# Kernel tuning notes

Hardware: AMD Instinct MI355X
Metric: run time of the kernel (lower is better)

The kernel has to match this reference:

```python
import jax, jax.numpy as jnp
import numpy as np

N, K, C, S = 40000, 16, 128, 8  # points, neighbors, channels, share_planes
EPS = 1e-5


def _bn(x, g, b, m, v):
    # eval-mode BatchNorm1d over the channel (last) axis
    return (x - m) * (g * jax.lax.rsqrt(v + EPS)) + b


def _forward(xyz, feats, Wq, bq, Wk, bk, Wv, bv, Wp1, bp1, p_gamma, p_beta, p_mean, p_var,
             Wp2, bp2, w_gamma, w_beta, w_mean, w_var, Ww1, bw1, w1_gamma, w1_beta,
             w1_mean, w1_var, Ww2, bw2, nei_ind):
    x = feats[0]          # (N, C)
    pos = xyz[0]          # (N, 3)
    idx = nei_ind[0]      # (N, K)

    q = x @ Wq + bq                      # (N, C)
    kf = (x @ Wk + bk)[idx]              # (N, K, C) neighbor gather
    vf = (x @ Wv + bv)[idx]              # (N, K, C)

    d = pos[idx] - pos[:, None, :]       # (N, K, 3) relative positions
    # linear_p: Linear_BN(3,3) -> ReLU -> Linear(3, C)
    p = jax.nn.relu(_bn(d @ Wp1 + bp1, p_gamma, p_beta, p_mean, p_var)) @ Wp2 + bp2  # (N, K, C)

    # mid_planes == out_planes, so the view(...,1,mid).sum(2) is an identity reshape
    w = kf - q[:, None, :] + p           # (N, K, C)
    w = _bn(w, w_gamma, w_beta, w_mean, w_var)  # bn_w over channels
    # linear_w: ReLU -> Linear_BN(C, C//S) -> ReLU -> Linear(C//S, C//S)
    w = jax.nn.relu(_bn(jax.nn.relu(w) @ Ww1 + bw1, w1_gamma, w1_beta, w1_mean, w1_var)) @ Ww2 + bw2  # (N, K, C//S)
    w = jax.nn.softmax(w, axis=1)        # softmax over K neighbors

    # grouped-channel weighted sum over neighbors
    agg = ((vf + p).reshape(N, K, S, C // S) * w[:, :, None, :]).sum(axis=1).reshape(N, C)

    # shortcut is Identity (in_planes == out_planes); broadcast over batch dim like torch
    return jax.nn.leaky_relu(agg[None, :, :] + feats, negative_slope=0.1)  # (1, N, C)


def setup_inputs() -> dict:
    key = jax.random.key(0)
    ks = jax.random.split(key, 16)
    f32 = jnp.float32

    def w(k, shape, scale):
        return jax.random.normal(k, shape, dtype=f32) * scale

    return {
        "xyz": jax.random.uniform(ks[0], (1, N, 3), dtype=f32),
        "feats": jax.random.normal(ks[1], (1, N, C), dtype=f32),
        "nei_ind": jax.random.randint(ks[2], (1, N, K), 0, N, dtype=jnp.int32),
        "Wq": w(ks[3], (C, C), C ** -0.5), "bq": jnp.zeros((C,), f32),
        "Wk": w(ks[4], (C, C), C ** -0.5), "bk": jnp.zeros((C,), f32),
        "Wv": w(ks[5], (C, C), C ** -0.5), "bv": jnp.zeros((C,), f32),
        "Wp1": w(ks[6], (3, 3), 0.5), "bp1": jnp.zeros((3,), f32),
        "p_gamma": jnp.ones((3,), f32), "p_beta": jnp.zeros((3,), f32),
        "p_mean": w(ks[7], (3,), 0.1), "p_var": jnp.ones((3,), f32),
        "Wp2": w(ks[8], (3, C), 0.5), "bp2": jnp.zeros((C,), f32),
        "w_gamma": jnp.ones((C,), f32), "w_beta": jnp.zeros((C,), f32),
        "w_mean": w(ks[9], (C,), 0.1), "w_var": jnp.ones((C,), f32),
        "Ww1": w(ks[10], (C, C // S), C ** -0.5), "bw1": jnp.zeros((C // S,), f32),
        "w1_gamma": jnp.ones((C // S,), f32), "w1_beta": jnp.zeros((C // S,), f32),
        "w1_mean": w(ks[11], (C // S,), 0.1), "w1_var": jnp.ones((C // S,), f32),
        "Ww2": w(ks[12], (C // S, C // S), (C // S) ** -0.5), "bw2": jnp.zeros((C // S,), f32),
    }


def reference(xyz, feats, nei_ind, Wq, bq, Wk, bk, Wv, bv, Wp1, bp1, p_gamma, p_beta,
              p_mean, p_var, Wp2, bp2, w_gamma, w_beta, w_mean, w_var, Ww1, bw1,
              w1_gamma, w1_beta, w1_mean, w1_var, Ww2, bw2):
    return _forward(xyz, feats, Wq, bq, Wk, bk, Wv, bv, Wp1, bp1, p_gamma, p_beta,
                    p_mean, p_var, Wp2, bp2, w_gamma, w_beta, w_mean, w_var, Ww1, bw1,
                    w1_gamma, w1_beta, w1_mean, w1_var, Ww2, bw2, nei_ind)
```

## Files before the change

### kernel.cpp

```cpp
#include <hip/hip_runtime.h>
#include <stdint.h>

#define N_PTS 40000
#define KNBR  16
#define CH    128
#define EPSV  1e-5f

typedef __attribute__((ext_vector_type(4))) float f32x4;
typedef __attribute__((ext_vector_type(8))) short bf16x8;

__device__ __forceinline__ float bf2f(ushort u) {
    union { uint32_t i; float f; } x; x.i = ((uint32_t)u) << 16; return x.f;
}
__device__ __forceinline__ float bflo(uint32_t u) {
    union { uint32_t i; float f; } x; x.i = u << 16; return x.f;
}
__device__ __forceinline__ float bfhi(uint32_t u) {
    union { uint32_t i; float f; } x; x.i = u & 0xffff0000u; return x.f;
}
__device__ __forceinline__ ushort f2bf(float f) {
    union { float f; uint32_t i; } x; x.f = f;
    uint32_t i = x.i;
    i += 0x7fffu + ((i >> 16) & 1u);
    return (ushort)(i >> 16);
}

#if __has_builtin(__builtin_amdgcn_cvt_pk_bf16_f32)
typedef __bf16 bf16x2v __attribute__((ext_vector_type(2)));
__device__ __forceinline__ uint32_t pack2(float a, float b) {
    union { bf16x2v v; uint32_t u; } x;
    x.v = __builtin_amdgcn_cvt_pk_bf16_f32(a, b);
    return x.u;
}
#else
__device__ __forceinline__ uint32_t pack2(float a, float b) {
    return (uint32_t)f2bf(a) | ((uint32_t)f2bf(b) << 16);
}
#endif

template <bool BF> struct IO;
template <> struct IO<true> {
    static __device__ __forceinline__ float  ld (const void* p, int i) { return bf2f(((const ushort*)p)[i]); }
    static __device__ __forceinline__ float2 ld2(const void* p, int i) { const uint32_t u = ((const uint32_t*)p)[i]; return make_float2(bflo(u), bfhi(u)); }
    static __device__ __forceinline__ ushort ldbf(const void* p, int i) { return ((const ushort*)p)[i]; }
    static __device__ __forceinline__ void   st2(void* p, int i, float a, float b) { ((uint32_t*)p)[i] = pack2(a, b); }
};
template <> struct IO<false> {
    static __device__ __forceinline__ float  ld (const void* p, int i) { return ((const float*)p)[i]; }
    static __device__ __forceinline__ float2 ld2(const void* p, int i) { return ((const float2*)p)[i]; }
    static __device__ __forceinline__ ushort ldbf(const void* p, int i) { return f2bf(((const float*)p)[i]); }
    static __device__ __forceinline__ void   st2(void* p, int i, float a, float b) { ((float2*)p)[i] = make_float2(a, b); }
};

__device__ __forceinline__ bool detect_bf16(const void* w_var) {
    return (*(const uint32_t*)w_var & 0xffffu) != 0u;
}

#define PROJ_BLOCKS 1250
template <bool BF>
__device__ void proj_body(
    const void* feats,
    const void* Wq, const void* bq, const void* Wk, const void* bk,
    const void* Wv, const void* bv,
    uint32_t* qws, uint4* kvws)
{
    const int l    = threadIdx.x & 63;
    const int w    = threadIdx.x >> 6;
    const int t    = l & 15;
    const int quad = l >> 4;
    const int cq   = w;

    const void* Wsrc[3] = { Wq, Wk, Wv };
    const void* bsrc[3] = { bq, bk, bv };

    bf16x8 afrag[3][4];
    float  bias[3][4];
    #pragma unroll
    for (int m = 0; m < 3; ++m) {
        #pragma unroll
        for (int s = 0; s < 4; ++s)
            #pragma unroll
            for (int j = 0; j < 8; ++j) {
                const int k = s * 32 + quad * 8 + j;
                afrag[m][s][j] = (short)IO<BF>::ldbf(Wsrc[m], k * CH + cq * 16 + t);
            }
        #pragma unroll
        for (int r = 0; r < 4; ++r)
            bias[m][r] = IO<BF>::ld(bsrc[m], cq * 16 + quad * 4 + r);
    }

    #pragma unroll
    for (int n = 0; n < 2; ++n) {
        const int tt = blockIdx.x + PROJ_BLOCKS * n;
        const int p0 = tt * 16;
        bf16x8 bfr[4];
        if (BF) {
            const ushort* xp = (const ushort*)feats + (p0 + t) * CH + quad * 8;
            #pragma unroll
            for (int s = 0; s < 4; ++s)
                bfr[s] = *(const bf16x8*)(xp + s * 32);
        } else {
            const float* xp = (const float*)feats + (p0 + t) * CH + quad * 8;
            #pragma unroll
            for (int s = 0; s < 4; ++s) {
                const float4 a = *(const float4*)(xp + s * 32);
                const float4 b = *(const float4*)(xp + s * 32 + 4);
                bfr[s][0] = (short)f2bf(a.x); bfr[s][1] = (short)f2bf(a.y);
                bfr[s][2] = (short)f2bf(a.z); bfr[s][3] = (short)f2bf(a.w);
                bfr[s][4] = (short)f2bf(b.x); bfr[s][5] = (short)f2bf(b.y);
                bfr[s][6] = (short)f2bf(b.z); bfr[s][7] = (short)f2bf(b.w);
            }
        }
        f32x4 acc[3];
        #pragma unroll
        for (int m = 0; m < 3; ++m) {
            acc[m] = f32x4{ bias[m][0], bias[m][1], bias[m][2], bias[m][3] };
            #pragma unroll
            for (int s = 0; s < 4; ++s)
                acc[m] = __builtin_amdgcn_mfma_f32_16x16x32_bf16(afrag[m][s], bfr[s], acc[m], 0, 0, 0);
        }
        const int p = p0 + t;
        const int m16 = cq * 4 + quad;
        uint2 qo;
        qo.x = pack2(acc[0][0], acc[0][1]);
        qo.y = pack2(acc[0][2], acc[0][3]);
        ((uint2*)qws)[p * 32 + m16] = qo;
        uint4 kv;
        kv.x = pack2(acc[1][0], acc[1][1]);
        kv.y = pack2(acc[2][0], acc[2][1]);
        kv.z = pack2(acc[1][2], acc[1][3]);
        kv.w = pack2(acc[2][2], acc[2][3]);
        kvws[p * 32 + m16] = kv;
    }
}

__global__ __launch_bounds__(512) void proj_kernel(
    const void* feats, const void* Wq, const void* bq, const void* Wk,
    const void* bk, const void* Wv, const void* bv, const void* w_var_probe,
    uint32_t* qws, uint4* kvws)
{
    if (detect_bf16(w_var_probe))
        proj_body<true >(feats, Wq, bq, Wk, bk, Wv, bv, qws, kvws);
    else
        proj_body<false>(feats, Wq, bq, Wk, bk, Wv, bv, qws, kvws);
}

template <bool BF>
__device__ void attn_body(
    const void* xyz, const void* feats, const int* __restrict__ nei,
    const uint32_t* __restrict__ qws, const uint2* __restrict__ kvws,
    const void* Wp1, const void* bp1, const void* p_gamma, const void* p_beta,
    const void* p_mean, const void* p_var, const void* Wp2, const void* bp2,
    const void* w_gamma, const void* w_beta, const void* w_mean, const void* w_var,
    const void* Ww1, const void* bw1, const void* w1_gamma, const void* w1_beta,
    const void* w1_mean, const void* w1_var, const void* Ww2, const void* bw2,
    void* out, ushort* wbuf, ushort* ubuf, float* wsm, float* hlds,
    int i0, int l)
{
    const int t = l & 15;
    const int quad = l >> 4;

    float A1[3][3], C1[3];
    #pragma unroll
    for (int b = 0; b < 3; ++b) {
        const float sb = IO<BF>::ld(p_gamma, b) * rsqrtf(IO<BF>::ld(p_var, b) + EPSV);
        C1[b] = (IO<BF>::ld(bp1, b) - IO<BF>::ld(p_mean, b)) * sb + IO<BF>::ld(p_beta, b);
        #pragma unroll
        for (int a = 0; a < 3; ++a) A1[a][b] = IO<BF>::ld(Wp1, a * 3 + b) * sb;
    }

    const float2 vg = IO<BF>::ld2(w_gamma, l);
    const float2 vb = IO<BF>::ld2(w_beta, l);
    const float2 vm = IO<BF>::ld2(w_mean, l);
    const float2 vv = IO<BF>::ld2(w_var, l);
    const float scw0 = vg.x * rsqrtf(vv.x + EPSV);
    const float scw1 = vg.y * rsqrtf(vv.y + EPSV);
    const float shw0 = vb.x - vm.x * scw0;
    const float shw1 = vb.y - vm.y * scw1;

    float wp2c[3][2];
    #pragma unroll
    for (int r = 0; r < 3; ++r) {
        const float2 u = IO<BF>::ld2(Wp2, r * 64 + l);
        wp2c[r][0] = u.x; wp2c[r][1] = u.y;
    }
    const float2 vbp2 = IO<BF>::ld2(bp2, l);
    const float bp20 = vbp2.x, bp21 = vbp2.y;

    bf16x8 bfrag1[4];
    #pragma unroll
    for (int s = 0; s < 4; ++s)
        #pragma unroll
        for (int kk = 0; kk < 8; ++kk) {
            const int k = s * 32 + quad * 8 + kk;
            bfrag1[s][kk] = (short)IO<BF>::ldbf(Ww1, k * 16 + t);
        }
    bf16x8 bfrag2;
    #pragma unroll
    for (int kk = 0; kk < 8; ++kk) {
        const int k = quad * 8 + kk;
        bfrag2[kk] = (quad < 2) ? (short)IO<BF>::ldbf(Ww2, k * 16 + t) : (short)0;
    }

    const float s1t  = IO<BF>::ld(w1_gamma, t) * rsqrtf(IO<BF>::ld(w1_var, t) + EPSV);
    const float sh1t = IO<BF>::ld(w1_beta, t) - IO<BF>::ld(w1_mean, t) * s1t;
    const float bw1t = IO<BF>::ld(bw1, t);
    const float bw2t = IO<BF>::ld(bw2, t);

    #pragma unroll 1
    for (int pp = 0; pp < 4; ++pp) {
        const int i = i0 + pp;

        const uint32_t uq = qws[i * 64 + l];
        const float qs0 = shw0 - bflo(uq) * scw0;
        const float qs1 = shw1 - bfhi(uq) * scw1;

        const float pix = IO<BF>::ld(xyz, i * 3 + 0);
        const float piy = IO<BF>::ld(xyz, i * 3 + 1);
        const float piz = IO<BF>::ld(xyz, i * 3 + 2);

        const int vnj = nei[i * KNBR + t];
        const float ndx = IO<BF>::ld(xyz, vnj * 3 + 0) - pix;
        const float ndy = IO<BF>::ld(xyz, vnj * 3 + 1) - piy;
        const float ndz = IO<BF>::ld(xyz, vnj * 3 + 2) - piz;
        const float hh0 = fmaxf(0.f, ndx * A1[0][0] + ndy * A1[1][0] + ndz * A1[2][0] + C1[0]);
        const float hh1 = fmaxf(0.f, ndx * A1[0][1] + ndy * A1[1][1] + ndz * A1[2][1] + C1[1]);
        const float hh2 = fmaxf(0.f, ndx * A1[0][2] + ndy * A1[1][2] + ndz * A1[2][2] + C1[2]);
        if (quad == 0)
            *(float4*)&hlds[t * 4] = make_float4(hh0, hh1, hh2, 0.f);

        int njs[KNBR];
        #pragma unroll
        for (int j = 0; j < KNBR; ++j) njs[j] = nei[i * KNBR + j];
        uint2 kv[KNBR];
        #pragma unroll
        for (int j = 0; j < KNBR; ++j) kv[j] = kvws[njs[j] * 64 + l];

        float vfp0[KNBR], vfp1[KNBR];
        #pragma unroll
        for (int j = 0; j < KNBR; ++j) {
            const float4 h = *(const float4*)&hlds[j * 4];
            const float p0 = h.x * wp2c[0][0] + h.y * wp2c[1][0] + h.z * wp2c[2][0] + bp20;
            const float p1 = h.x * wp2c[0][1] + h.y * wp2c[1][1] + h.z * wp2c[2][1] + bp21;
            vfp0[j] = bflo(kv[j].y) + p0;
            vfp1[j] = bfhi(kv[j].y) + p1;
            const float w0 = fmaxf(0.f, fmaf(bflo(kv[j].x) + p0, scw0, qs0));
            const float w1 = fmaxf(0.f, fmaf(bfhi(kv[j].x) + p1, scw1, qs1));
            ((uint32_t*)wbuf)[j * 68 + l] = pack2(w0, w1);
        }

        f32x4 acc1 = { bw1t, bw1t, bw1t, bw1t };
        const ushort* arow = &wbuf[t * 136 + quad * 8];
        #pragma unroll
        for (int s = 0; s < 4; ++s) {
            const bf16x8 afrag = *(const bf16x8*)(arow + s * 32);
            acc1 = __builtin_amdgcn_mfma_f32_16x16x32_bf16(afrag, bfrag1[s], acc1, 0, 0, 0);
        }
        #pragma unroll
        for (int r = 0; r < 4; ++r) {
            const float u = fmaxf(0.f, acc1[r] * s1t + sh1t);
            ubuf[(quad * 4 + r) * 24 + t] = f2bf(u);
        }

        f32x4 acc2 = { bw2t, bw2t, bw2t, bw2t };
        bf16x8 afrag2;
        if (quad < 2) {
            afrag2 = *(const bf16x8*)(&ubuf[t * 24 + quad * 8]);
        } else {
            #pragma unroll
            for (int kk = 0; kk < 8; ++kk) afrag2[kk] = 0;
        }
        acc2 = __builtin_amdgcn_mfma_f32_16x16x32_bf16(afrag2, bfrag2, acc2, 0, 0, 0);

        float z0 = acc2[0], z1 = acc2[1], z2 = acc2[2], z3 = acc2[3];
        float mx = fmaxf(fmaxf(z0, z1), fmaxf(z2, z3));
        mx = fmaxf(mx, __shfl_xor(mx, 16));
        mx = fmaxf(mx, __shfl_xor(mx, 32));
        const float e0 = __expf(z0 - mx), e1 = __expf(z1 - mx);
        const float e2 = __expf(z2 - mx), e3 = __expf(z3 - mx);
        float ssum = e0 + e1 + e2 + e3;
        ssum += __shfl_xor(ssum, 16);
        ssum += __shfl_xor(ssum, 32);
        const float inv = 1.0f / ssum;
        wsm[(quad * 4 + 0) * 18 + t] = e0 * inv;
        wsm[(quad * 4 + 1) * 18 + t] = e1 * inv;
        wsm[(quad * 4 + 2) * 18 + t] = e2 * inv;
        wsm[(quad * 4 + 3) * 18 + t] = e3 * inv;

        const int t0 = (2 * l) & 15;
        float agg0 = 0.f, agg1 = 0.f;
        #pragma unroll
        for (int j = 0; j < KNBR; ++j) {
            const float2 wp = *(const float2*)&wsm[j * 18 + t0];
            agg0 = fmaf(vfp0[j], wp.x, agg0);
            agg1 = fmaf(vfp1[j], wp.y, agg1);
        }
        const float2 xf = IO<BF>::ld2(feats, i * 64 + l);
        float o0 = agg0 + xf.x;
        float o1 = agg1 + xf.y;
        o0 = o0 > 0.f ? o0 : 0.1f * o0;
        o1 = o1 > 0.f ? o1 : 0.1f * o1;
        IO<BF>::st2(out, i * 64 + l, o0, o1);
    }
}

__global__ __launch_bounds__(256) void attn_kernel(
    const void* xyz, const void* feats, const int* __restrict__ nei,
    const uint32_t* __restrict__ qws, const uint2* __restrict__ kvws,
    const void* Wp1, const void* bp1, const void* p_gamma, const void* p_beta,
    const void* p_mean, const void* p_var, const void* Wp2, const void* bp2,
    const void* w_gamma, const void* w_beta, const void* w_mean, const void* w_var,
    const void* Ww1, const void* bw1, const void* w1_gamma, const void* w1_beta,
    const void* w1_mean, const void* w1_var, const void* Ww2, const void* bw2,
    void* out)
{
    __shared__ ushort wbuf[4][16 * 136];
    __shared__ ushort ubuf[4][16 * 24];
    __shared__ float  wsm [4][16 * 18];
    __shared__ float  hlds[4][16 * 4];

    const int wave = threadIdx.x >> 6;
    const int l    = threadIdx.x & 63;
    const int i0   = blockIdx.x * 16 + wave * 4;

    if (detect_bf16(w_var))
        attn_body<true >(xyz, feats, nei, qws, kvws, Wp1, bp1, p_gamma, p_beta,
                         p_mean, p_var, Wp2, bp2, w_gamma, w_beta, w_mean, w_var,
                         Ww1, bw1, w1_gamma, w1_beta, w1_mean, w1_var, Ww2, bw2,
                         out, wbuf[wave], ubuf[wave], wsm[wave], hlds[wave], i0, l);
    else
        attn_body<false>(xyz, feats, nei, qws, kvws, Wp1, bp1, p_gamma, p_beta,
                         p_mean, p_var, Wp2, bp2, w_gamma, w_beta, w_mean, w_var,
                         Ww1, bw1, w1_gamma, w1_beta, w1_mean, w1_var, Ww2, bw2,
                         out, wbuf[wave], ubuf[wave], wsm[wave], hlds[wave], i0, l);
}

extern "C" void kernel_launch(void* const* d_in, const int* in_sizes, int n_in,
                              void* d_out, int out_size, void* d_ws, size_t ws_size,
                              hipStream_t stream) {
    const void* xyz     = d_in[0];
    const void* feats   = d_in[1];
    const int*  nei     = (const int*)d_in[2];
    const void* Wq      = d_in[3];
    const void* bq      = d_in[4];
    const void* Wk      = d_in[5];
    const void* bk      = d_in[6];
    const void* Wv      = d_in[7];
    const void* bv      = d_in[8];
    const void* Wp1     = d_in[9];
    const void* bp1     = d_in[10];
    const void* p_gamma = d_in[11];
    const void* p_beta  = d_in[12];
    const void* p_mean  = d_in[13];
    const void* p_var   = d_in[14];
    const void* Wp2     = d_in[15];
    const void* bp2     = d_in[16];
    const void* w_gamma = d_in[17];
    const void* w_beta  = d_in[18];
    const void* w_mean  = d_in[19];
    const void* w_var   = d_in[20];
    const void* Ww1     = d_in[21];
    const void* bw1     = d_in[22];
    const void* w1_gamma= d_in[23];
    const void* w1_beta = d_in[24];
    const void* w1_mean = d_in[25];
    const void* w1_var  = d_in[26];
    const void* Ww2     = d_in[27];
    const void* bw2     = d_in[28];

    uint32_t* qws  = (uint32_t*)d_ws;
    uint4*    kvws = (uint4*)(qws + (size_t)N_PTS * 64);

    proj_kernel<<<PROJ_BLOCKS, 512, 0, stream>>>(feats, Wq, bq, Wk, bk, Wv, bv, w_var,
                                                 qws, kvws);
    attn_kernel<<<N_PTS / 16, 256, 0, stream>>>(xyz, feats, nei, qws, (const uint2*)kvws,
                                          Wp1, bp1, p_gamma, p_beta, p_mean, p_var,
                                          Wp2, bp2, w_gamma, w_beta, w_mean, w_var,
                                          Ww1, bw1, w1_gamma, w1_beta, w1_mean, w1_var,
                                          Ww2, bw2, d_out);
}
```

Baseline: 224.9 us.

## Software-pipeline neighbor gathers across points in attention kernel

Loads the next point's query, position, neighbor indices and gathered K/V rows while the current point runs its MFMA and softmax stages, so the irregular gathers overlap with compute instead of stalling at the top of each iteration. Neighbor indices are broadcast with readlane from the per-lane index register instead of 16 scalar index loads. The residual feature load is moved earlier and restrict qualifiers are added. Holding the prefetched K/V rows alive across the loop raises register pressure, which may cut occupancy.

```diff
diff --git a/kernel.cpp b/kernel.cpp
--- a/kernel.cpp
+++ b/kernel.cpp
@@ -147,14 +147,15 @@
 
 template <bool BF>
 __device__ void attn_body(
-    const void* xyz, const void* feats, const int* __restrict__ nei,
+    const void* __restrict__ xyz, const void* __restrict__ feats,
+    const int* __restrict__ nei,
     const uint32_t* __restrict__ qws, const uint2* __restrict__ kvws,
     const void* Wp1, const void* bp1, const void* p_gamma, const void* p_beta,
     const void* p_mean, const void* p_var, const void* Wp2, const void* bp2,
     const void* w_gamma, const void* w_beta, const void* w_mean, const void* w_var,
     const void* Ww1, const void* bw1, const void* w1_gamma, const void* w1_beta,
     const void* w1_mean, const void* w1_var, const void* Ww2, const void* bw2,
-    void* out, ushort* wbuf, ushort* ubuf, float* wsm, float* hlds,
+    void* __restrict__ out, ushort* wbuf, ushort* ubuf, float* wsm, float* hlds,
     int i0, int l)
 {
     const int t = l & 15;
@@ -207,46 +208,76 @@
     const float bw1t = IO<BF>::ld(bw1, t);
     const float bw2t = IO<BF>::ld(bw2, t);
 
+    uint32_t uqA;
+    float pixA, piyA, pizA;
+    float nxA, nyA, nzA;
+    uint2 kvA[KNBR];
+
+    {
+        uqA  = qws[i0 * 64 + l];
+        pixA = IO<BF>::ld(xyz, i0 * 3 + 0);
+        piyA = IO<BF>::ld(xyz, i0 * 3 + 1);
+        pizA = IO<BF>::ld(xyz, i0 * 3 + 2);
+        const int vnj = nei[i0 * KNBR + t];
+        nxA = IO<BF>::ld(xyz, vnj * 3 + 0);
+        nyA = IO<BF>::ld(xyz, vnj * 3 + 1);
+        nzA = IO<BF>::ld(xyz, vnj * 3 + 2);
+        #pragma unroll
+        for (int j = 0; j < KNBR; ++j) {
+            const int nj = __builtin_amdgcn_readlane(vnj, j);
+            kvA[j] = kvws[(size_t)nj * 64 + l];
+        }
+    }
+
     #pragma unroll 1
     for (int pp = 0; pp < 4; ++pp) {
         const int i = i0 + pp;
-
-        const uint32_t uq = qws[i * 64 + l];
-        const float qs0 = shw0 - bflo(uq) * scw0;
-        const float qs1 = shw1 - bfhi(uq) * scw1;
-
-        const float pix = IO<BF>::ld(xyz, i * 3 + 0);
-        const float piy = IO<BF>::ld(xyz, i * 3 + 1);
-        const float piz = IO<BF>::ld(xyz, i * 3 + 2);
-
-        const int vnj = nei[i * KNBR + t];
-        const float ndx = IO<BF>::ld(xyz, vnj * 3 + 0) - pix;
-        const float ndy = IO<BF>::ld(xyz, vnj * 3 + 1) - piy;
-        const float ndz = IO<BF>::ld(xyz, vnj * 3 + 2) - piz;
+        const int inext = i + 1;
+
+        const float qs0 = shw0 - bflo(uqA) * scw0;
+        const float qs1 = shw1 - bfhi(uqA) * scw1;
+        const float ndx = nxA - pixA;
+        const float ndy = nyA - piyA;
+        const float ndz = nzA - pizA;
+
+        int vnj2 = 0;
+        if (pp < 3) {
+            uqA  = qws[inext * 64 + l];
+            pixA = IO<BF>::ld(xyz, inext * 3 + 0);
+            piyA = IO<BF>::ld(xyz, inext * 3 + 1);
+            pizA = IO<BF>::ld(xyz, inext * 3 + 2);
+            vnj2 = nei[inext * KNBR + t];
+        }
+        const float2 xf = IO<BF>::ld2(feats, i * 64 + l);
+
         const float hh0 = fmaxf(0.f, ndx * A1[0][0] + ndy * A1[1][0] + ndz * A1[2][0] + C1[0]);
         const float hh1 = fmaxf(0.f, ndx * A1[0][1] + ndy * A1[1][1] + ndz * A1[2][1] + C1[1]);
         const float hh2 = fmaxf(0.f, ndx * A1[0][2] + ndy * A1[1][2] + ndz * A1[2][2] + C1[2]);
         if (quad == 0)
             *(float4*)&hlds[t * 4] = make_float4(hh0, hh1, hh2, 0.f);
 
-        int njs[KNBR];
-        #pragma unroll
-        for (int j = 0; j < KNBR; ++j) njs[j] = nei[i * KNBR + j];
-        uint2 kv[KNBR];
-        #pragma unroll
-        for (int j = 0; j < KNBR; ++j) kv[j] = kvws[njs[j] * 64 + l];
-
         float vfp0[KNBR], vfp1[KNBR];
         #pragma unroll
         for (int j = 0; j < KNBR; ++j) {
             const float4 h = *(const float4*)&hlds[j * 4];
             const float p0 = h.x * wp2c[0][0] + h.y * wp2c[1][0] + h.z * wp2c[2][0] + bp20;
             const float p1 = h.x * wp2c[0][1] + h.y * wp2c[1][1] + h.z * wp2c[2][1] + bp21;
-            vfp0[j] = bflo(kv[j].y) + p0;
-            vfp1[j] = bfhi(kv[j].y) + p1;
-            const float w0 = fmaxf(0.f, fmaf(bflo(kv[j].x) + p0, scw0, qs0));
-            const float w1 = fmaxf(0.f, fmaf(bfhi(kv[j].x) + p1, scw1, qs1));
+            vfp0[j] = bflo(kvA[j].y) + p0;
+            vfp1[j] = bfhi(kvA[j].y) + p1;
+            const float w0 = fmaxf(0.f, fmaf(bflo(kvA[j].x) + p0, scw0, qs0));
+            const float w1 = fmaxf(0.f, fmaf(bfhi(kvA[j].x) + p1, scw1, qs1));
             ((uint32_t*)wbuf)[j * 68 + l] = pack2(w0, w1);
+        }
+
+        if (pp < 3) {
+            nxA = IO<BF>::ld(xyz, vnj2 * 3 + 0);
+            nyA = IO<BF>::ld(xyz, vnj2 * 3 + 1);
+            nzA = IO<BF>::ld(xyz, vnj2 * 3 + 2);
+            #pragma unroll
+            for (int j = 0; j < KNBR; ++j) {
+                const int nj = __builtin_amdgcn_readlane(vnj2, j);
+                kvA[j] = kvws[(size_t)nj * 64 + l];
+            }
         }
 
         f32x4 acc1 = { bw1t, bw1t, bw1t, bw1t };
@@ -295,7 +326,6 @@
             agg0 = fmaf(vfp0[j], wp.x, agg0);
             agg1 = fmaf(vfp1[j], wp.y, agg1);
         }
-        const float2 xf = IO<BF>::ld2(feats, i * 64 + l);
         float o0 = agg0 + xf.x;
         float o1 = agg1 + xf.y;
         o0 = o0 > 0.f ? o0 : 0.1f * o0;
@@ -305,14 +335,15 @@
 }
 
 __global__ __launch_bounds__(256) void attn_kernel(
-    const void* xyz, const void* feats, const int* __restrict__ nei,
+    const void* __restrict__ xyz, const void* __restrict__ feats,
+    const int* __restrict__ nei,
     const uint32_t* __restrict__ qws, const uint2* __restrict__ kvws,
     const void* Wp1, const void* bp1, const void* p_gamma, const void* p_beta,
     const void* p_mean, const void* p_var, const void* Wp2, const void* bp2,
     const void* w_gamma, const void* w_beta, const void* w_mean, const void* w_var,
     const void* Ww1, const void* bw1, const void* w1_gamma, const void* w1_beta,
     const void* w1_mean, const void* w1_var, const void* Ww2, const void* bw2,
-    void* out)
+    void* __restrict__ out)
 {
     __shared__ ushort wbuf[4][16 * 136];
     __shared__ ushort ubuf[4][16 * 24];
```

Result: slower. 229.8 us (+2.2%).

## Factor positional term out of value aggregation and defer value gather

Applied to the files above, without the earlier changes.

Uses linearity of the positional encoding so that sum_j w_j*(v_j+p_j) becomes sum_j w_j*v_j + Wp2·(sum_j w_j*h_j) + bp2. The softmax-weighted hidden sums are computed once in shared memory. The value gather is split from the key gather and issued after the key computation, so 16 value registers are no longer held across the MLP. Shared memory is merged into one aliased per-wave buffer, and uniform constants are hoisted to scalar registers via readfirstlane. Register pressure drops, which could raise occupancy, at the cost of two narrower 4-byte gathers per neighbour instead of one 8-byte gather.

```diff
diff --git a/kernel.cpp b/kernel.cpp
--- a/kernel.cpp
+++ b/kernel.cpp
@@ -23,6 +23,12 @@
     uint32_t i = x.i;
     i += 0x7fffu + ((i >> 16) & 1u);
     return (ushort)(i >> 16);
+}
+
+__device__ __forceinline__ float rfl(float x) {
+    union { float f; int i; } u; u.f = x;
+    u.i = __builtin_amdgcn_readfirstlane(u.i);
+    return u.f;
 }
 
 #if __has_builtin(__builtin_amdgcn_cvt_pk_bf16_f32)
@@ -147,14 +153,15 @@
 
 template <bool BF>
 __device__ void attn_body(
-    const void* xyz, const void* feats, const int* __restrict__ nei,
-    const uint32_t* __restrict__ qws, const uint2* __restrict__ kvws,
+    const void* __restrict__ xyz, const void* __restrict__ feats,
+    const int* __restrict__ nei,
+    const uint32_t* __restrict__ qws, const uint32_t* __restrict__ kvw,
     const void* Wp1, const void* bp1, const void* p_gamma, const void* p_beta,
     const void* p_mean, const void* p_var, const void* Wp2, const void* bp2,
     const void* w_gamma, const void* w_beta, const void* w_mean, const void* w_var,
     const void* Ww1, const void* bw1, const void* w1_gamma, const void* w1_beta,
     const void* w1_mean, const void* w1_var, const void* Ww2, const void* bw2,
-    void* out, ushort* wbuf, ushort* ubuf, float* wsm, float* hlds,
+    void* __restrict__ out, ushort* wbuf, ushort* ubuf, float* wsm, float* Sb,
     int i0, int l)
 {
     const int t = l & 15;
@@ -164,9 +171,9 @@
     #pragma unroll
     for (int b = 0; b < 3; ++b) {
         const float sb = IO<BF>::ld(p_gamma, b) * rsqrtf(IO<BF>::ld(p_var, b) + EPSV);
-        C1[b] = (IO<BF>::ld(bp1, b) - IO<BF>::ld(p_mean, b)) * sb + IO<BF>::ld(p_beta, b);
-        #pragma unroll
-        for (int a = 0; a < 3; ++a) A1[a][b] = IO<BF>::ld(Wp1, a * 3 + b) * sb;
+        C1[b] = rfl((IO<BF>::ld(bp1, b) - IO<BF>::ld(p_mean, b)) * sb + IO<BF>::ld(p_beta, b));
+        #pragma unroll
+        for (int a = 0; a < 3; ++a) A1[a][b] = rfl(IO<BF>::ld(Wp1, a * 3 + b) * sb);
     }
 
     const float2 vg = IO<BF>::ld2(w_gamma, l);
@@ -218,8 +225,7 @@
         const float pix = IO<BF>::ld(xyz, i * 3 + 0);
         const float piy = IO<BF>::ld(xyz, i * 3 + 1);
         const float piz = IO<BF>::ld(xyz, i * 3 + 2);
-
-        const int vnj = nei[i * KNBR + t];
+        const int   vnj = nei[i * KNBR + t];
         const float ndx = IO<BF>::ld(xyz, vnj * 3 + 0) - pix;
         const float ndy = IO<BF>::ld(xyz, vnj * 3 + 1) - piy;
         const float ndz = IO<BF>::ld(xyz, vnj * 3 + 2) - piz;
@@ -227,27 +233,37 @@
         const float hh1 = fmaxf(0.f, ndx * A1[0][1] + ndy * A1[1][1] + ndz * A1[2][1] + C1[1]);
         const float hh2 = fmaxf(0.f, ndx * A1[0][2] + ndy * A1[1][2] + ndz * A1[2][2] + C1[2]);
         if (quad == 0)
-            *(float4*)&hlds[t * 4] = make_float4(hh0, hh1, hh2, 0.f);
-
-        int njs[KNBR];
-        #pragma unroll
-        for (int j = 0; j < KNBR; ++j) njs[j] = nei[i * KNBR + j];
-        uint2 kv[KNBR];
-        #pragma unroll
-        for (int j = 0; j < KNBR; ++j) kv[j] = kvws[njs[j] * 64 + l];
-
-        float vfp0[KNBR], vfp1[KNBR];
-        #pragma unroll
-        for (int j = 0; j < KNBR; ++j) {
-            const float4 h = *(const float4*)&hlds[j * 4];
-            const float p0 = h.x * wp2c[0][0] + h.y * wp2c[1][0] + h.z * wp2c[2][0] + bp20;
-            const float p1 = h.x * wp2c[0][1] + h.y * wp2c[1][1] + h.z * wp2c[2][1] + bp21;
-            vfp0[j] = bflo(kv[j].y) + p0;
-            vfp1[j] = bfhi(kv[j].y) + p1;
-            const float w0 = fmaxf(0.f, fmaf(bflo(kv[j].x) + p0, scw0, qs0));
-            const float w1 = fmaxf(0.f, fmaf(bfhi(kv[j].x) + p1, scw1, qs1));
-            ((uint32_t*)wbuf)[j * 68 + l] = pack2(w0, w1);
-        }
+            *(float4*)&wbuf[t * 136 + 128] = make_float4(hh0, hh1, hh2, 0.f);
+
+        {
+            int njs[KNBR];
+            #pragma unroll
+            for (int j = 0; j < KNBR; ++j) njs[j] = nei[i * KNBR + j];
+            uint32_t kA[KNBR];
+            #pragma unroll
+            for (int j = 0; j < KNBR; ++j)
+                kA[j] = kvw[(size_t)njs[j] * 128 + 2 * l];
+
+            #pragma unroll
+            for (int j = 0; j < KNBR; ++j) {
+                const float4 h = *(const float4*)&wbuf[j * 136 + 128];
+                const float p0 = h.x * wp2c[0][0] + h.y * wp2c[1][0] + h.z * wp2c[2][0] + bp20;
+                const float p1 = h.x * wp2c[0][1] + h.y * wp2c[1][1] + h.z * wp2c[2][1] + bp21;
+                const float w0 = fmaxf(0.f, fmaf(bflo(kA[j]) + p0, scw0, qs0));
+                const float w1 = fmaxf(0.f, fmaf(bfhi(kA[j]) + p1, scw1, qs1));
+                ((uint32_t*)wbuf)[j * 68 + l] = pack2(w0, w1);
+            }
+        }
+
+        uint32_t vB[KNBR];
+        {
+            int i2 = i;
+            asm volatile("" : "+v"(i2));
+            #pragma unroll
+            for (int j = 0; j < KNBR; ++j)
+                vB[j] = kvw[(size_t)nei[i2 * KNBR + j] * 128 + 2 * l + 1];
+        }
+        const float2 xf = IO<BF>::ld2(feats, i * 64 + l);
 
         f32x4 acc1 = { bw1t, bw1t, bw1t, bw1t };
         const ushort* arow = &wbuf[t * 136 + quad * 8];
@@ -282,20 +298,34 @@
         ssum += __shfl_xor(ssum, 16);
         ssum += __shfl_xor(ssum, 32);
         const float inv = 1.0f / ssum;
-        wsm[(quad * 4 + 0) * 18 + t] = e0 * inv;
-        wsm[(quad * 4 + 1) * 18 + t] = e1 * inv;
-        wsm[(quad * 4 + 2) * 18 + t] = e2 * inv;
-        wsm[(quad * 4 + 3) * 18 + t] = e3 * inv;
+        wsm[(quad * 4 + 0) * 17 + t] = e0 * inv;
+        wsm[(quad * 4 + 1) * 17 + t] = e1 * inv;
+        wsm[(quad * 4 + 2) * 17 + t] = e2 * inv;
+        wsm[(quad * 4 + 3) * 17 + t] = e3 * inv;
+
+        if (quad < 3) {
+            float s = 0.f;
+            #pragma unroll
+            for (int j = 0; j < KNBR; ++j)
+                s = fmaf(((const float*)&wbuf[j * 136 + 128])[quad], wsm[j * 17 + t], s);
+            Sb[quad * 16 + t] = s;
+        }
 
         const int t0 = (2 * l) & 15;
         float agg0 = 0.f, agg1 = 0.f;
         #pragma unroll
         for (int j = 0; j < KNBR; ++j) {
-            const float2 wp = *(const float2*)&wsm[j * 18 + t0];
-            agg0 = fmaf(vfp0[j], wp.x, agg0);
-            agg1 = fmaf(vfp1[j], wp.y, agg1);
-        }
-        const float2 xf = IO<BF>::ld2(feats, i * 64 + l);
+            const float wq0 = wsm[j * 17 + t0];
+            const float wq1 = wsm[j * 17 + t0 + 1];
+            agg0 = fmaf(bflo(vB[j]), wq0, agg0);
+            agg1 = fmaf(bfhi(vB[j]), wq1, agg1);
+        }
+        #pragma unroll
+        for (int a = 0; a < 3; ++a) {
+            agg0 = fmaf(wp2c[a][0], Sb[a * 16 + t0],     agg0);
+            agg1 = fmaf(wp2c[a][1], Sb[a * 16 + t0 + 1], agg1);
+        }
+        agg0 += bp20; agg1 += bp21;
         float o0 = agg0 + xf.x;
         float o1 = agg1 + xf.y;
         o0 = o0 > 0.f ? o0 : 0.1f * o0;
@@ -305,34 +335,38 @@
 }
 
 __global__ __launch_bounds__(256) void attn_kernel(
-    const void* xyz, const void* feats, const int* __restrict__ nei,
-    const uint32_t* __restrict__ qws, const uint2* __restrict__ kvws,
+    const void* __restrict__ xyz, const void* __restrict__ feats,
+    const int* __restrict__ nei,
+    const uint32_t* __restrict__ qws, const uint32_t* __restrict__ kvw,
     const void* Wp1, const void* bp1, const void* p_gamma, const void* p_beta,
     const void* p_mean, const void* p_var, const void* Wp2, const void* bp2,
     const void* w_gamma, const void* w_beta, const void* w_mean, const void* w_var,
     const void* Ww1, const void* bw1, const void* w1_gamma, const void* w1_beta,
     const void* w1_mean, const void* w1_var, const void* Ww2, const void* bw2,
-    void* out)
+    void* __restrict__ out)
 {
-    __shared__ ushort wbuf[4][16 * 136];
-    __shared__ ushort ubuf[4][16 * 24];
-    __shared__ float  wsm [4][16 * 18];
-    __shared__ float  hlds[4][16 * 4];
+    __shared__ unsigned char smem[4][5648];
 
     const int wave = threadIdx.x >> 6;
     const int l    = threadIdx.x & 63;
     const int i0   = blockIdx.x * 16 + wave * 4;
 
+    ushort* wbuf = (ushort*)&smem[wave][0];
+    float*  uw   = (float*)&smem[wave][4352];
+    ushort* ubuf = (ushort*)uw;
+    float*  wsm  = uw;
+    float*  Sb   = uw + 272;
+
     if (detect_bf16(w_var))
-        attn_body<true >(xyz, feats, nei, qws, kvws, Wp1, bp1, p_gamma, p_beta,
+        attn_body<true >(xyz, feats, nei, qws, kvw, Wp1, bp1, p_gamma, p_beta,
                          p_mean, p_var, Wp2, bp2, w_gamma, w_beta, w_mean, w_var,
                          Ww1, bw1, w1_gamma, w1_beta, w1_mean, w1_var, Ww2, bw2,
-                         out, wbuf[wave], ubuf[wave], wsm[wave], hlds[wave], i0, l);
+                         out, wbuf, ubuf, wsm, Sb, i0, l);
     else
-        attn_body<false>(xyz, feats, nei, qws, kvws, Wp1, bp1, p_gamma, p_beta,
+        attn_body<false>(xyz, feats, nei, qws, kvw, Wp1, bp1, p_gamma, p_beta,
                          p_mean, p_var, Wp2, bp2, w_gamma, w_beta, w_mean, w_var,
                          Ww1, bw1, w1_gamma, w1_beta, w1_mean, w1_var, Ww2, bw2,
-                         out, wbuf[wave], ubuf[wave], wsm[wave], hlds[wave], i0, l);
+                         out, wbuf, ubuf, wsm, Sb, i0, l);
 }
 
 extern "C" void kernel_launch(void* const* d_in, const int* in_sizes, int n_in,
@@ -373,7 +407,8 @@
 
     proj_kernel<<<PROJ_BLOCKS, 512, 0, stream>>>(feats, Wq, bq, Wk, bk, Wv, bv, w_var,
                                                  qws, kvws);
-    attn_kernel<<<N_PTS / 16, 256, 0, stream>>>(xyz, feats, nei, qws, (const uint2*)kvws,
+    attn_kernel<<<N_PTS / 16, 256, 0, stream>>>(xyz, feats, nei, qws,
+                                          (const uint32_t*)kvws,
                                           Wp1, bp1, p_gamma, p_beta, p_mean, p_var,
                                           Wp2, bp2, w_gamma, w_beta, w_mean, w_var,
                                           Ww1, bw1, w1_gamma, w1_beta, w1_mean, w1_var,
```

Measured after the change: 241.0 us. +7.1%, slower.
